# Kernel tuning notes

Measured on AMD Instinct MI355X. Metric: run time of the kernel, lower is better.

Reference implementation:

```python
import jax, jax.numpy as jnp
import numpy as np

B_, T_, D_MODEL = 2, 1024, 1024
D_STATE, D_CONV, EXPAND = 16, 4, 2
D_INNER = D_MODEL * EXPAND


def setup_inputs() -> dict:
    key = jax.random.key(0)
    ks = jax.random.split(key, 12)
    def s(k, shape, sc=0.02):
        return jax.random.normal(k, shape, jnp.float32) * sc
    return {
        "x": jax.random.normal(ks[0], (B_, T_, D_MODEL), jnp.float32),
        "ln_g": jnp.ones((D_MODEL,), jnp.float32),
        "ln_b": jnp.zeros((D_MODEL,), jnp.float32),
        "W_in": s(ks[1], (D_MODEL, 2 * D_INNER)),
        "b_in": s(ks[2], (2 * D_INNER,)),
        "conv_w": s(ks[3], (D_INNER, 1, D_CONV)),  # depthwise kernel, torch OIH layout
        "conv_b": s(ks[4], (D_INNER,)),
        "A": s(ks[5], (D_INNER, D_STATE), 0.1),
        "W_B": s(ks[6], (D_INNER, D_STATE)),
        "b_B": s(ks[7], (D_STATE,)),
        "W_C": s(ks[8], (D_INNER, D_STATE)),
        "b_C": s(ks[9], (D_STATE,)),
        "D": jnp.ones((D_INNER,), jnp.float32),
        "W_out": s(ks[10], (D_INNER, D_MODEL)),
        "b_out": s(ks[11], (D_MODEL,)),
    }


def _ssm_forward(x, ln_g, ln_b, W_in, b_in, conv_w, conv_b, A, W_B, b_B, W_C, b_C, D, W_out, b_out):
    eps = 1e-5
    # LayerNorm (biased variance, as in torch)
    mu = jnp.mean(x, axis=-1, keepdims=True)
    var = jnp.var(x, axis=-1, keepdims=True)
    xn = (x - mu) / jnp.sqrt(var + eps) * ln_g + ln_b
    # in_proj -> split into x path and gate
    proj = xn @ W_in + b_in                      # (b, t, 2*d_inner)
    xp, gate = jnp.split(proj, 2, axis=-1)
    # depthwise causal conv1d (padding=d_conv-1 on the left == torch pad + truncate)
    xc = jax.lax.conv_general_dilated(
        xp.transpose(0, 2, 1), conv_w,
        window_strides=(1,), padding=[(D_CONV - 1, 0)],
        dimension_numbers=("NCH", "OIH", "NCH"),
        feature_group_count=D_INNER,
    ).transpose(0, 2, 1) + conv_b                # (b, t, d_inner)
    xc = jax.nn.silu(xc)
    Bt = xc @ W_B + b_B                          # (b, t, d_state)
    Ct = xc @ W_C + b_C                          # (b, t, d_state)
    a = jax.nn.sigmoid(A)                        # (d_inner, d_state), per-channel decay
    u = Bt[:, :, None, :] * xc[:, :, :, None]    # (b, t, d_inner, d_state)
    a_full = jnp.broadcast_to(a, u.shape)
    # h_t = a * h_{t-1} + u_t  via first-order-recurrence associative scan
    def combine(c1, c2):
        a1, u1 = c1
        a2, u2 = c2
        return a2 * a1, a2 * u1 + u2
    _, h = jax.lax.associative_scan(combine, (a_full, u), axis=1)
    y = jnp.einsum("btns,bts->btn", h, Ct) + D * xc
    y = y * jax.nn.silu(gate)
    return y @ W_out + b_out + x                 # residual (dropout is identity in eval)


def reference(x, ln_g, ln_b, W_in, b_in, conv_w, conv_b, A, W_B, b_B, W_C, b_C, D, W_out, b_out):
    return _ssm_forward(x, ln_g, ln_b, W_in, b_in, conv_w, conv_b, A, W_B, b_B, W_C, b_C, D, W_out, b_out)
```

## Files before the change

### kernel.cpp

```cpp
#include <hip/hip_runtime.h>
#include <hip/hip_bf16.h>
#include <stdint.h>

using u16 = unsigned short;
typedef short bf16x8 __attribute__((ext_vector_type(8)));
typedef float f32x4 __attribute__((ext_vector_type(4)));

__device__ __forceinline__ float b2f(u16 u) {
  union { unsigned int i; float f; } v; v.i = ((unsigned int)u) << 16; return v.f;
}
__device__ __forceinline__ u16 f2b(float f) {
  __hip_bfloat16 h = __float2bfloat16(f);
  u16 r; __builtin_memcpy(&r, &h, 2); return r;
}
__device__ __forceinline__ bool probe_bf16(const void* p) {
  return *(const unsigned int*)p == 0x3F803F80u;
}
__device__ __forceinline__ float loadf(const void* p, size_t i, bool bf) {
  return bf ? b2f(((const u16*)p)[i]) : ((const float*)p)[i];
}
__device__ __forceinline__ void gload_lds16(const u16* g, u16* l) {
  __builtin_amdgcn_global_load_lds(
      (const __attribute__((address_space(1))) unsigned int*)(g),
      (__attribute__((address_space(3))) unsigned int*)(l),
      16, 0, 0);
}
template <int BK>
__device__ __forceinline__ int swkey(int row) {
  if constexpr (BK == 32) return (row >> 1) & 3;
  else return row & (BK / 8 - 1);
}

__global__ void transpose_any_k(const void* __restrict__ in, u16* __restrict__ out,
                                int R, int C, const void* __restrict__ probe) {
  const bool bf = probe_bf16(probe);
  __shared__ u16 tile[32][33];
  int c0 = blockIdx.x * 32, r0 = blockIdx.y * 32;
  int tx = threadIdx.x, ty = threadIdx.y;
#pragma unroll
  for (int i = 0; i < 4; i++) {
    size_t idx = (size_t)(r0 + ty + i * 8) * C + c0 + tx;
    tile[ty + i * 8][tx] = bf ? ((const u16*)in)[idx] : f2b(((const float*)in)[idx]);
  }
  __syncthreads();
#pragma unroll
  for (int i = 0; i < 4; i++)
    out[(size_t)(c0 + ty + i * 8) * R + r0 + tx] = tile[tx][ty + i * 8];
}

__launch_bounds__(256)
__global__ void ln_kernel(const void* __restrict__ x, const void* __restrict__ g,
                          const void* __restrict__ b, u16* __restrict__ xn) {
  const bool bf = probe_bf16(g);
  const int row = blockIdx.x, tid = threadIdx.x;
  const size_t base = (size_t)row * 1024;
  float v[4]; float s = 0.f, s2 = 0.f;
#pragma unroll
  for (int i = 0; i < 4; i++) {
    v[i] = loadf(x, base + tid + i * 256, bf);
    s += v[i]; s2 += v[i] * v[i];
  }
#pragma unroll
  for (int m = 32; m >= 1; m >>= 1) { s += __shfl_xor(s, m); s2 += __shfl_xor(s2, m); }
  __shared__ float rs[4], rs2[4];
  if ((tid & 63) == 0) { rs[tid >> 6] = s; rs2[tid >> 6] = s2; }
  __syncthreads();
  s = rs[0] + rs[1] + rs[2] + rs[3];
  s2 = rs2[0] + rs2[1] + rs2[2] + rs2[3];
  float mu = s * (1.f / 1024.f);
  float var = s2 * (1.f / 1024.f) - mu * mu;
  float rstd = rsqrtf(var + 1e-5f);
#pragma unroll
  for (int i = 0; i < 4; i++) {
    int c = tid + i * 256;
    float o = (v[i] - mu) * rstd * loadf(g, c, bf) + loadf(b, c, bf);
    xn[base + c] = f2b(o);
  }
}

template <int ROWS, int BK>
__device__ __forceinline__ void stage_tile(const u16* __restrict__ g, u16* lbuf,
                                           int K, int wave, int lane) {
  constexpr int LPR = BK / 8;
  constexpr int RPI = 512 / BK;
  constexpr int NI = ROWS / RPI;
  const int lr = lane / LPR, lc = lane % LPR;
#pragma unroll
  for (int j = wave; j < NI; j += 4) {
    int row = j * RPI + lr;
    int col = (lc ^ swkey<BK>(row)) * 8;
    gload_lds16(g + (size_t)row * K + col, lbuf + (size_t)j * RPI * BK);
  }
}

template <int BM, int BN, int BK, bool RESID, bool DUALOUT>
__launch_bounds__(256)
__global__ void gemm_async(const u16* __restrict__ A, const u16* __restrict__ BT,
                           const void* __restrict__ bias, const void* __restrict__ resid,
                           void* __restrict__ Cout, int M, int N, int K,
                           const void* __restrict__ probe) {
  constexpr int WM = BM / 2, WN = BN / 2;
  constexpr int TM = WM / 16, TN = WN / 16;
  constexpr int KF = BK / 32;
  __shared__ __align__(16) u16 lds[2][(BM + BN) * BK];
  const int tid = threadIdx.x;
  const int bm = blockIdx.x, bn = blockIdx.y;
  const int lane = tid & 63, wave = tid >> 6;
  const int wm = wave >> 1, wn = wave & 1;
  const int lrow = lane & 15, quad = lane >> 4;
  f32x4 acc[TM][TN] = {};
  const u16* Ag = A + (size_t)bm * BM * K;
  const u16* Bg = BT + (size_t)bn * BN * K;

  stage_tile<BM, BK>(Ag, &lds[0][0], K, wave, lane);
  stage_tile<BN, BK>(Bg, &lds[0][BM * BK], K, wave, lane);
  __syncthreads();

  int cur = 0;
  for (int k0 = 0; k0 < K; k0 += BK, cur ^= 1) {
    if (k0 + BK < K) {
      stage_tile<BM, BK>(Ag + k0 + BK, &lds[cur ^ 1][0], K, wave, lane);
      stage_tile<BN, BK>(Bg + k0 + BK, &lds[cur ^ 1][BM * BK], K, wave, lane);
    }
    const u16* bufA = &lds[cur][0];
    const u16* bufB = &lds[cur][BM * BK];
#pragma unroll
    for (int f = 0; f < KF; f++) {
      bf16x8 af[TM], bv[TN];
#pragma unroll
      for (int i = 0; i < TM; i++) {
        int row = wm * WM + i * 16 + lrow;
        af[i] = *(const bf16x8*)&bufA[(size_t)row * BK + (((f * 4 + quad) ^ swkey<BK>(row)) * 8)];
      }
#pragma unroll
      for (int j = 0; j < TN; j++) {
        int row = wn * WN + j * 16 + lrow;
        bv[j] = *(const bf16x8*)&bufB[(size_t)row * BK + (((f * 4 + quad) ^ swkey<BK>(row)) * 8)];
      }
#pragma unroll
      for (int i = 0; i < TM; i++)
#pragma unroll
        for (int j = 0; j < TN; j++)
          acc[i][j] = __builtin_amdgcn_mfma_f32_16x16x32_bf16(af[i], bv[j], acc[i][j], 0, 0, 0);
    }
    __syncthreads();
  }

  const bool bf = probe_bf16(probe);
#pragma unroll
  for (int i = 0; i < TM; i++) {
#pragma unroll
    for (int j = 0; j < TN; j++) {
      int col = bn * BN + wn * WN + j * 16 + lrow;
      float bvv = loadf(bias, col, bf);
#pragma unroll
      for (int r = 0; r < 4; r++) {
        int row = bm * BM + wm * WM + i * 16 + quad * 4 + r;
        float v = acc[i][j][r] + bvv;
        if constexpr (RESID) v += loadf(resid, (size_t)row * N + col, bf);
        if constexpr (DUALOUT) {
          if (bf) ((u16*)Cout)[(size_t)row * N + col] = f2b(v);
          else    ((float*)Cout)[(size_t)row * N + col] = v;
        } else {
          ((u16*)Cout)[(size_t)row * N + col] = f2b(v);
        }
      }
    }
  }
}

__global__ void conv_silu_kernel(const u16* __restrict__ proj, const void* __restrict__ cw,
                                 const void* __restrict__ cb, u16* __restrict__ xc,
                                 const void* __restrict__ probe) {
  const bool bf = probe_bf16(probe);
  const int n = blockIdx.x * 256 + threadIdx.x;
  const int row = blockIdx.y;
  const int t = row & 1023;
  float w[4];
#pragma unroll
  for (int k = 0; k < 4; k++) w[k] = loadf(cw, n * 4 + k, bf);
  float s = loadf(cb, n, bf);
#pragma unroll
  for (int k = 0; k < 4; k++) {
    int tt = t - 3 + k;
    if (tt >= 0) s += b2f(proj[(size_t)(row - 3 + k) * 4096 + n]) * w[k];
  }
  float sg = 1.f / (1.f + __expf(-s));
  xc[(size_t)row * 2048 + n] = f2b(s * sg);
}

__launch_bounds__(256)
__global__ void bc_proj_kernel(const u16* __restrict__ xc, const void* __restrict__ WB,
                               const void* __restrict__ bB, const void* __restrict__ WC,
                               const void* __restrict__ bC, float* __restrict__ BC,
                               const void* __restrict__ probe) {
  const bool bf = probe_bf16(probe);
  __shared__ float xr[2112];
  __shared__ float red[8][33];
  const int row = blockIdx.x, tid = threadIdx.x;
  const u16* xp = xc + (size_t)row * 2048;
  {
    int k0 = tid * 8;
    union { int4 v; u16 u[8]; } uu;
    uu.v = *(const int4*)(xp + k0);
    int base = k0 + (k0 >> 5);
#pragma unroll
    for (int e = 0; e < 8; e++) xr[base + e] = b2f(uu.u[e]);
  }
  __syncthreads();
  const int c = tid & 31, sl = tid >> 5, cc = c & 15;
  const void* W = (c < 16) ? WB : WC;
  float p = 0.f;
  int k = sl * 256;
  if (bf) {
    const u16* W16 = (const u16*)W;
#pragma unroll 8
    for (int kk = 0; kk < 256; kk++, k++)
      p = __builtin_fmaf(xr[k + (k >> 5)], b2f(W16[k * 16 + cc]), p);
  } else {
    const float* W32 = (const float*)W;
#pragma unroll 8
    for (int kk = 0; kk < 256; kk++, k++)
      p = __builtin_fmaf(xr[k + (k >> 5)], W32[k * 16 + cc], p);
  }
  red[sl][c] = p;
  __syncthreads();
  if (tid < 32) {
    float s = 0.f;
#pragma unroll
    for (int i = 0; i < 8; i++) s += red[i][tid];
    s += (tid < 16) ? loadf(bB, tid, bf) : loadf(bC, tid - 16, bf);
    BC[(size_t)row * 32 + tid] = s;
  }
}


__launch_bounds__(256)
__global__ void scan_pass1(const u16* __restrict__ xc, const float* __restrict__ BC,
                           const void* __restrict__ Abuf, float* __restrict__ carry,
                           const void* __restrict__ probe) {
  const bool bf = probe_bf16(probe);
  const int tid = threadIdx.x;
  const int c = blockIdx.x & 15, ng = (blockIdx.x >> 4) & 7, bi = blockIdx.x >> 7;
  const int n = ng * 256 + tid;
  float a[16], h[16];
#pragma unroll
  for (int s = 0; s < 16; s++) {
    float av = loadf(Abuf, n * 16 + s, bf);
    a[s] = 1.f / (1.f + __expf(-av));
    h[s] = 0.f;
  }
  __shared__ __align__(16) u16 xs[32 * 256];
  __shared__ __align__(16) float bcs[32 * 32];
  const u16* xcp = xc + (size_t)bi * 1024 * 2048 + ng * 256;
  const float* bcp = BC + (size_t)bi * 1024 * 32;
  for (int half = 0; half < 2; half++) {
    const int tc = c * 64 + half * 32;
    __syncthreads();
#pragma unroll
    for (int i = 0; i < 4; i++) {
      int ch = tid + i * 256;
      int r = ch >> 5, cv = (ch & 31) * 8;
      *(int4*)&xs[ch * 8] = *(const int4*)(xcp + (size_t)(tc + r) * 2048 + cv);
    }
    {
      int r = tid >> 3, cv = (tid & 7) * 4;
      *(int4*)&bcs[tid * 4] = *(const int4*)(bcp + (size_t)(tc + r) * 32 + cv);
    }
    __syncthreads();
    for (int t = 0; t < 32; t++) {
      float x = b2f(xs[t * 256 + tid]);
#pragma unroll
      for (int s = 0; s < 16; s++)
        h[s] = __builtin_fmaf(a[s], h[s], bcs[t * 32 + s] * x);
    }
  }
  float* cp = carry + ((size_t)(bi * 16 + c) * 2048 + n) * 16;
#pragma unroll
  for (int s = 0; s < 16; s++) cp[s] = h[s];
}

__launch_bounds__(256)
__global__ void scan_prefix(float* __restrict__ carry, const void* __restrict__ Abuf,
                            const void* __restrict__ probe) {
  const bool bf = probe_bf16(probe);
  const int g = blockIdx.x * 256 + threadIdx.x;
  const int s = g & 15, n = (g >> 4) & 2047, bi = g >> 15;
  float a = 1.f / (1.f + __expf(-loadf(Abuf, n * 16 + s, bf)));
  float aL = a;
#pragma unroll
  for (int i = 0; i < 6; i++) aL = aL * aL;
  float running = 0.f;
  for (int c = 0; c < 16; c++) {
    size_t idx = ((size_t)(bi * 16 + c) * 2048 + n) * 16 + s;
    float tmp = carry[idx];
    carry[idx] = running;
    running = __builtin_fmaf(aL, running, tmp);
  }
}

__launch_bounds__(256)
__global__ void scan_pass2(const u16* __restrict__ xc, const u16* __restrict__ proj,
                           const float* __restrict__ BC, const void* __restrict__ Abuf,
                           const void* __restrict__ Dbuf, const float* __restrict__ carry,
                           u16* __restrict__ ybar, const void* __restrict__ probe) {
  const bool bf = probe_bf16(probe);
  const int tid = threadIdx.x;
  const int c = blockIdx.x & 15, ng = (blockIdx.x >> 4) & 7, bi = blockIdx.x >> 7;
  const int n = ng * 256 + tid;
  float a[16], h[16];
  const float* cp = carry + ((size_t)(bi * 16 + c) * 2048 + n) * 16;
#pragma unroll
  for (int s = 0; s < 16; s++) {
    float av = loadf(Abuf, n * 16 + s, bf);
    a[s] = 1.f / (1.f + __expf(-av));
    h[s] = cp[s];
  }
  const float Dn = loadf(Dbuf, n, bf);
  __shared__ __align__(16) u16 xs[32 * 256];
  __shared__ __align__(16) u16 gs[32 * 256];
  __shared__ __align__(16) float bcs[32 * 32];
  const u16* xcp = xc + (size_t)bi * 1024 * 2048 + ng * 256;
  const u16* gp = proj + (size_t)bi * 1024 * 4096 + 2048 + ng * 256;
  const float* bcp = BC + (size_t)bi * 1024 * 32;
  u16* yp = ybar + (size_t)bi * 1024 * 2048 + ng * 256;
  for (int half = 0; half < 2; half++) {
    const int tc = c * 64 + half * 32;
    __syncthreads();
#pragma unroll
    for (int i = 0; i < 4; i++) {
      int ch = tid + i * 256;
      int r = ch >> 5, cv = (ch & 31) * 8;
      *(int4*)&xs[ch * 8] = *(const int4*)(xcp + (size_t)(tc + r) * 2048 + cv);
      *(int4*)&gs[ch * 8] = *(const int4*)(gp + (size_t)(tc + r) * 4096 + cv);
    }
    {
      int r = tid >> 3, cv = (tid & 7) * 4;
      *(int4*)&bcs[tid * 4] = *(const int4*)(bcp + (size_t)(tc + r) * 32 + cv);
    }
    __syncthreads();
    for (int t = 0; t < 32; t++) {
      float x = b2f(xs[t * 256 + tid]);
      float acc = 0.f;
#pragma unroll
      for (int s = 0; s < 16; s++) {
        h[s] = __builtin_fmaf(a[s], h[s], bcs[t * 32 + s] * x);
        acc = __builtin_fmaf(h[s], bcs[t * 32 + 16 + s], acc);
      }
      float y = acc + Dn * x;
      float g = b2f(gs[t * 256 + tid]);
      float yg = y * g / (1.f + __expf(-g));
      yp[(size_t)(tc + t) * 2048 + tid] = f2b(yg);
    }
  }
}

extern "C" void kernel_launch(void* const* d_in, const int* in_sizes, int n_in,
                              void* d_out, int out_size, void* d_ws, size_t ws_size,
                              hipStream_t stream) {
  const void* x = d_in[0];
  const void* ln_g = d_in[1];
  const void* ln_b = d_in[2];
  const void* W_in = d_in[3];
  const void* b_in = d_in[4];
  const void* conv_w = d_in[5];
  const void* conv_b = d_in[6];
  const void* A = d_in[7];
  const void* W_B = d_in[8];
  const void* b_B = d_in[9];
  const void* W_C = d_in[10];
  const void* b_C = d_in[11];
  const void* Dp = d_in[12];
  const void* W_out = d_in[13];
  const void* b_out = d_in[14];
  const void* probe = ln_g;

  char* ws = (char*)d_ws;
  u16* WinT = (u16*)ws;
  u16* ybar = (u16*)ws;
  u16* xn = (u16*)(ws + (size_t)8 * 1024 * 1024);
  u16* WoutT = xn;
  u16* proj = (u16*)(ws + (size_t)12 * 1024 * 1024);
  u16* xcb = (u16*)(ws + (size_t)28 * 1024 * 1024);
  float* BC = (float*)(ws + (size_t)36 * 1024 * 1024);
  float* carry = (float*)(ws + (size_t)36 * 1024 * 1024 + 256 * 1024);

  transpose_any_k<<<dim3(128, 32), dim3(32, 8), 0, stream>>>(W_in, WinT, 1024, 4096, probe);
  ln_kernel<<<2048, 256, 0, stream>>>(x, ln_g, ln_b, xn);
  gemm_async<128, 128, 32, false, false><<<dim3(16, 32), 256, 0, stream>>>(
      xn, WinT, b_in, nullptr, proj, 2048, 4096, 1024, probe);
  transpose_any_k<<<dim3(32, 64), dim3(32, 8), 0, stream>>>(W_out, WoutT, 2048, 1024, probe);
  conv_silu_kernel<<<dim3(8, 2048), 256, 0, stream>>>(proj, conv_w, conv_b, xcb, probe);
  bc_proj_kernel<<<2048, 256, 0, stream>>>(xcb, W_B, b_B, W_C, b_C, BC, probe);
  scan_pass1<<<256, 256, 0, stream>>>(xcb, BC, A, carry, probe);
  scan_prefix<<<256, 256, 0, stream>>>(carry, A, probe);
  scan_pass2<<<256, 256, 0, stream>>>(xcb, proj, BC, A, Dp, carry, ybar, probe);
  gemm_async<128, 64, 64, true, true><<<dim3(16, 16), 256, 0, stream>>>(
      ybar, WoutT, b_out, x, d_out, 2048, 1024, 2048, probe);
}
```

Measured before the change: 244.8 us.

## Fuse conv+SiLU into B/C projection, split-K output GEMM, widen in_proj BK

Merges the depthwise causal conv and SiLU into the B/C projection kernel, so xc is computed once per row, kept in LDS and written once, and the separate reread of xc is gone. The output projection GEMM now uses split-K with two K halves written as fp32 partials to workspace, followed by a reduction kernel that adds bias and residual. This doubles the block count of a 256-block GEMM to fill more CUs. The in_proj GEMM's K tile grows from 32 to 64. The costs are extra fp32 partial traffic, one more launch, and more LDS use per block in the in_proj GEMM.

Result: slower. 256.3 us (+4.7%).

```diff
diff --git a/kernel.cpp b/kernel.cpp
--- a/kernel.cpp
+++ b/kernel.cpp
@@ -93,32 +93,33 @@
   }
 }
 
-template <int BM, int BN, int BK, bool RESID, bool DUALOUT>
+template <int BM, int BN, int BK, bool RESID, bool DUALOUT, bool PARTIAL>
 __launch_bounds__(256)
 __global__ void gemm_async(const u16* __restrict__ A, const u16* __restrict__ BT,
                            const void* __restrict__ bias, const void* __restrict__ resid,
-                           void* __restrict__ Cout, int M, int N, int K,
+                           void* __restrict__ Cout, float* __restrict__ Cpart,
+                           int M, int N, int K, int k_len,
                            const void* __restrict__ probe) {
   constexpr int WM = BM / 2, WN = BN / 2;
   constexpr int TM = WM / 16, TN = WN / 16;
   constexpr int KF = BK / 32;
   __shared__ __align__(16) u16 lds[2][(BM + BN) * BK];
   const int tid = threadIdx.x;
-  const int bm = blockIdx.x, bn = blockIdx.y;
+  const int bm = blockIdx.x, bn = blockIdx.y, bz = blockIdx.z;
   const int lane = tid & 63, wave = tid >> 6;
   const int wm = wave >> 1, wn = wave & 1;
   const int lrow = lane & 15, quad = lane >> 4;
   f32x4 acc[TM][TN] = {};
-  const u16* Ag = A + (size_t)bm * BM * K;
-  const u16* Bg = BT + (size_t)bn * BN * K;
+  const u16* Ag = A + (size_t)bm * BM * K + (size_t)bz * k_len;
+  const u16* Bg = BT + (size_t)bn * BN * K + (size_t)bz * k_len;
 
   stage_tile<BM, BK>(Ag, &lds[0][0], K, wave, lane);
   stage_tile<BN, BK>(Bg, &lds[0][BM * BK], K, wave, lane);
   __syncthreads();
 
   int cur = 0;
-  for (int k0 = 0; k0 < K; k0 += BK, cur ^= 1) {
-    if (k0 + BK < K) {
+  for (int k0 = 0; k0 < k_len; k0 += BK, cur ^= 1) {
+    if (k0 + BK < k_len) {
       stage_tile<BM, BK>(Ag + k0 + BK, &lds[cur ^ 1][0], K, wave, lane);
       stage_tile<BN, BK>(Bg + k0 + BK, &lds[cur ^ 1][BM * BK], K, wave, lane);
     }
@@ -144,6 +145,22 @@
           acc[i][j] = __builtin_amdgcn_mfma_f32_16x16x32_bf16(af[i], bv[j], acc[i][j], 0, 0, 0);
     }
     __syncthreads();
+  }
+
+  if constexpr (PARTIAL) {
+    float* P = Cpart + (size_t)bz * M * N;
+#pragma unroll
+    for (int i = 0; i < TM; i++)
+#pragma unroll
+      for (int j = 0; j < TN; j++) {
+        int col = bn * BN + wn * WN + j * 16 + lrow;
+#pragma unroll
+        for (int r = 0; r < 4; r++) {
+          int row = bm * BM + wm * WM + i * 16 + quad * 4 + r;
+          P[(size_t)row * N + col] = acc[i][j][r];
+        }
+      }
+    return;
   }
 
   const bool bf = probe_bf16(probe);
@@ -169,43 +186,66 @@
   }
 }
 
-__global__ void conv_silu_kernel(const u16* __restrict__ proj, const void* __restrict__ cw,
-                                 const void* __restrict__ cb, u16* __restrict__ xc,
-                                 const void* __restrict__ probe) {
-  const bool bf = probe_bf16(probe);
-  const int n = blockIdx.x * 256 + threadIdx.x;
-  const int row = blockIdx.y;
-  const int t = row & 1023;
-  float w[4];
-#pragma unroll
-  for (int k = 0; k < 4; k++) w[k] = loadf(cw, n * 4 + k, bf);
-  float s = loadf(cb, n, bf);
-#pragma unroll
-  for (int k = 0; k < 4; k++) {
-    int tt = t - 3 + k;
-    if (tt >= 0) s += b2f(proj[(size_t)(row - 3 + k) * 4096 + n]) * w[k];
-  }
-  float sg = 1.f / (1.f + __expf(-s));
-  xc[(size_t)row * 2048 + n] = f2b(s * sg);
-}
-
-__launch_bounds__(256)
-__global__ void bc_proj_kernel(const u16* __restrict__ xc, const void* __restrict__ WB,
+__launch_bounds__(256)
+__global__ void reduce_out(const float* __restrict__ p, const void* __restrict__ bias,
+                           const void* __restrict__ resid, void* __restrict__ out,
+                           const void* __restrict__ probe) {
+  const bool bf = probe_bf16(probe);
+  const int row = blockIdx.x, c0 = threadIdx.x * 4;
+  const size_t i = (size_t)row * 1024 + c0;
+  f32x4 a = *(const f32x4*)(p + i);
+  f32x4 b = *(const f32x4*)(p + (size_t)2048 * 1024 + i);
+  float o[4];
+#pragma unroll
+  for (int e = 0; e < 4; e++)
+    o[e] = a[e] + b[e] + loadf(bias, c0 + e, bf) + loadf(resid, i + e, bf);
+  if (bf) {
+    u16 pk[4];
+#pragma unroll
+    for (int e = 0; e < 4; e++) pk[e] = f2b(o[e]);
+    *(uint2*)((u16*)out + i) = *(uint2*)pk;
+  } else {
+    f32x4 v; v[0] = o[0]; v[1] = o[1]; v[2] = o[2]; v[3] = o[3];
+    *(f32x4*)((float*)out + i) = v;
+  }
+}
+
+__launch_bounds__(256)
+__global__ void conv_bc_kernel(const u16* __restrict__ proj, const void* __restrict__ cw,
+                               const void* __restrict__ cb, const void* __restrict__ WB,
                                const void* __restrict__ bB, const void* __restrict__ WC,
-                               const void* __restrict__ bC, float* __restrict__ BC,
-                               const void* __restrict__ probe) {
+                               const void* __restrict__ bC, u16* __restrict__ xcb,
+                               float* __restrict__ BC, const void* __restrict__ probe) {
   const bool bf = probe_bf16(probe);
   __shared__ float xr[2112];
   __shared__ float red[8][33];
   const int row = blockIdx.x, tid = threadIdx.x;
-  const u16* xp = xc + (size_t)row * 2048;
+  const int t = row & 1023;
+  const int n0 = tid * 8;
+  float acc[8];
+#pragma unroll
+  for (int e = 0; e < 8; e++) acc[e] = loadf(cb, n0 + e, bf);
+#pragma unroll
+  for (int k = 0; k < 4; k++) {
+    if (t - 3 + k >= 0) {
+      union { int4 v; u16 u[8]; } uu;
+      uu.v = *(const int4*)(proj + (size_t)(row - 3 + k) * 4096 + n0);
+#pragma unroll
+      for (int e = 0; e < 8; e++)
+        acc[e] = __builtin_fmaf(b2f(uu.u[e]), loadf(cw, (n0 + e) * 4 + k, bf), acc[e]);
+    }
+  }
   {
-    int k0 = tid * 8;
-    union { int4 v; u16 u[8]; } uu;
-    uu.v = *(const int4*)(xp + k0);
-    int base = k0 + (k0 >> 5);
-#pragma unroll
-    for (int e = 0; e < 8; e++) xr[base + e] = b2f(uu.u[e]);
+    union { int4 v; u16 u[8]; } pk;
+    int base = n0 + (n0 >> 5);
+#pragma unroll
+    for (int e = 0; e < 8; e++) {
+      float s = acc[e];
+      float xv = s / (1.f + __expf(-s));
+      xr[base + e] = xv;
+      pk.u[e] = f2b(xv);
+    }
+    *(int4*)(xcb + (size_t)row * 2048 + n0) = pk.v;
   }
   __syncthreads();
   const int c = tid & 31, sl = tid >> 5, cc = c & 15;
@@ -384,17 +424,19 @@
   u16* xcb = (u16*)(ws + (size_t)28 * 1024 * 1024);
   float* BC = (float*)(ws + (size_t)36 * 1024 * 1024);
   float* carry = (float*)(ws + (size_t)36 * 1024 * 1024 + 256 * 1024);
+  float* part = (float*)(ws + (size_t)48 * 1024 * 1024);
 
   transpose_any_k<<<dim3(128, 32), dim3(32, 8), 0, stream>>>(W_in, WinT, 1024, 4096, probe);
   ln_kernel<<<2048, 256, 0, stream>>>(x, ln_g, ln_b, xn);
-  gemm_async<128, 128, 32, false, false><<<dim3(16, 32), 256, 0, stream>>>(
-      xn, WinT, b_in, nullptr, proj, 2048, 4096, 1024, probe);
+  gemm_async<128, 128, 64, false, false, false><<<dim3(16, 32), 256, 0, stream>>>(
+      xn, WinT, b_in, nullptr, proj, nullptr, 2048, 4096, 1024, 1024, probe);
   transpose_any_k<<<dim3(32, 64), dim3(32, 8), 0, stream>>>(W_out, WoutT, 2048, 1024, probe);
-  conv_silu_kernel<<<dim3(8, 2048), 256, 0, stream>>>(proj, conv_w, conv_b, xcb, probe);
-  bc_proj_kernel<<<2048, 256, 0, stream>>>(xcb, W_B, b_B, W_C, b_C, BC, probe);
+  conv_bc_kernel<<<2048, 256, 0, stream>>>(proj, conv_w, conv_b, W_B, b_B, W_C, b_C,
+                                           xcb, BC, probe);
   scan_pass1<<<256, 256, 0, stream>>>(xcb, BC, A, carry, probe);
   scan_prefix<<<256, 256, 0, stream>>>(carry, A, probe);
   scan_pass2<<<256, 256, 0, stream>>>(xcb, proj, BC, A, Dp, carry, ybar, probe);
-  gemm_async<128, 64, 64, true, true><<<dim3(16, 16), 256, 0, stream>>>(
-      ybar, WoutT, b_out, x, d_out, 2048, 1024, 2048, probe);
-}
+  gemm_async<128, 64, 64, false, false, true><<<dim3(16, 16, 2), 256, 0, stream>>>(
+      ybar, WoutT, nullptr, nullptr, nullptr, part, 2048, 1024, 2048, 1024, probe);
+  reduce_out<<<2048, 256, 0, stream>>>(part, b_out, x, d_out, probe);
+}
```
